# Kernel optimization log

Hardware: AMD Instinct MI355X
Metric: run time of the kernel (lower is better)

Reference implementation:

```python
import jax, jax.numpy as jnp
import numpy as np

N_PATHS, SEQ_LEN = 8192, 512
DATA_DIM, HIDDEN = 2, 128
MIN_VOL, MAX_VOL = 1e-4, 5.0


def setup_inputs() -> dict:
    key = jax.random.key(0)
    ks = jax.random.split(key, 10)
    def w(k, fin, fout, scale=1.0):
        return (jax.random.normal(k, (fin, fout), jnp.float32) * (scale / np.sqrt(fin))).astype(jnp.float32)
    # diffusion output bias init from the torch module: log(exp(target_vol) - 1 + 1e-8)
    gb3_init = float(np.log(np.exp(0.1) - 1.0 + 1e-8))
    return {
        "y0": jax.random.normal(ks[0], (N_PATHS, DATA_DIM), jnp.float32) * 0.1,
        "ts": jnp.arange(SEQ_LEN, dtype=jnp.float32),  # dt = 1.0 between outputs
        "dW": jax.random.normal(ks[1], (SEQ_LEN - 1, N_PATHS, DATA_DIM), jnp.float32),
        "fw1": w(ks[2], DATA_DIM + 1, HIDDEN), "fb1": jnp.zeros((HIDDEN,), jnp.float32),
        "fw2": w(ks[3], HIDDEN, HIDDEN),       "fb2": jnp.zeros((HIDDEN,), jnp.float32),
        "fw3": w(ks[4], HIDDEN, DATA_DIM, 0.02), "fb3": jnp.zeros((DATA_DIM,), jnp.float32),
        "gw1": w(ks[5], DATA_DIM, HIDDEN),     "gb1": jnp.zeros((HIDDEN,), jnp.float32),
        "gw2": w(ks[6], HIDDEN, HIDDEN),       "gb2": jnp.zeros((HIDDEN,), jnp.float32),
        "gw3": w(ks[7], HIDDEN, DATA_DIM, 0.02),
        "gb3": jnp.full((DATA_DIM,), gb3_init, jnp.float32),
    }


def _sde_paths(y0, ts, dW, fw1, fb1, fw2, fb2, fw3, fb3, gw1, gb1, gw2, gb2, gw3, gb3):
    def drift(y):  # f(t, y): MLP on [y, spread]
        spread = y[:, 0:1] - y[:, 1:2]
        h = jnp.concatenate([y, spread], axis=-1)            # [N, D+1]
        h = jax.nn.silu(h @ fw1 + fb1)
        h = jax.nn.silu(h @ fw2 + fb2)
        return h @ fw3 + fb3                                  # [N, D]

    def diffusion(y):  # g(t, y): softplus + clamp
        h = jax.nn.silu(y @ gw1 + gb1)
        h = jax.nn.silu(h @ gw2 + gb2)
        raw = h @ gw3 + gb3
        return jnp.clip(jax.nn.softplus(raw), MIN_VOL, MAX_VOL)  # [N, D]

    dts = ts[1:] - ts[:-1]  # [T-1]

    def step(y, inp):
        dw_std, dt = inp
        dw = dw_std * jnp.sqrt(dt)                 # Brownian increment ~ N(0, dt)
        f = drift(y)
        g, vjp_g = jax.vjp(diffusion, y)
        v = 0.5 * (dw * dw - dt)                   # Milstein weight (Ito)
        corr = vjp_g(v * g)[0]                     # torchsde autograd gdg_prod
        y1 = y + f * dt + g * dw + corr
        return y1, y1

    _, ys = jax.lax.scan(step, y0, (dW, dts))      # ys: [T-1, N, D]
    paths = jnp.concatenate([y0[None], ys], axis=0)  # [T, N, D]
    return jnp.transpose(paths, (1, 0, 2))           # [N, T, D]


def reference(y0, ts, dW, fw1, fb1, fw2, fb2, fw3, fb3, gw1, gb1, gw2, gb2, gw3, gb3):
    return _sde_paths(y0, ts, dW, fw1, fb1, fw2, fb2, fw3, fb3,
                      gw1, gb1, gw2, gb2, gw3, gb3)
```

## Files before the change

kernel.cpp:

```cpp
#include <hip/hip_runtime.h>
#include <math.h>

#define H      128
#define NPATH  8192
#define TLEN   512
#define BP     32
#define NTHR   512

typedef short bf16x8 __attribute__((ext_vector_type(8)));
typedef float f32x4  __attribute__((ext_vector_type(4)));

#define MFMA(a,b,c) __builtin_amdgcn_mfma_f32_16x16x32_bf16((a),(b),(c),0,0,0)

#define O_WF2T  0
#define O_WG2T  (O_WF2T + 32768)
#define O_WG2R  (O_WG2T + 32768)
#define O_BFH   (O_WG2R + 32768)
#define O_BFL   (O_BFH + 8192)
#define O_BGH   (O_BFL + 8192)
#define O_BGL   (O_BGH + 8192)
#define O_PF    (O_BGL + 8192)
#define O_PRAW  (O_PF   + 1024)
#define O_PCORR (O_PRAW + 1024)
#define O_TS    (O_PCORR+ 1024)
#define SMEM_BYTES (O_TS + TLEN*4)

__device__ __forceinline__ float bf2f(unsigned v){ return __uint_as_float(v << 16); }
__device__ __forceinline__ unsigned short f2bf(float f){
  unsigned u = __float_as_uint(f);
  return (unsigned short)((u + 0x7fffu + ((u >> 16) & 1u)) >> 16);
}
__device__ __forceinline__ float ldany(const void* p, long long i, bool isbf){
  return isbf ? bf2f(((const unsigned short*)p)[i]) : ((const float*)p)[i];
}
__device__ __forceinline__ unsigned short ldbf(const void* p, long long i, bool isbf){
  return isbf ? ((const unsigned short*)p)[i] : f2bf(((const float*)p)[i]);
}
__device__ __forceinline__ float fsig(float x){
  return __builtin_amdgcn_rcpf(1.0f + __expf(-x));
}
__device__ __forceinline__ float fsilu(float x){ return x * fsig(x); }
__device__ __forceinline__ float fsilud(float x){
  float s = fsig(x); return s * (1.0f + x * (1.0f - s));
}
__device__ __forceinline__ float fsoftplus(float x){
  if (x > 15.0f) return x;
  return __logf(1.0f + __expf(x));
}
__device__ __forceinline__ void split2(float x, unsigned short& hi, unsigned short& lo){
  unsigned short h = f2bf(x);
  hi = h;
  lo = f2bf(x - bf2f(h));
}
__device__ __forceinline__ int physB(int row, int col){
  return (row << 8) + ((((col >> 3) ^ (row & 15)) << 4) | ((col & 7) << 1));
}
__device__ __forceinline__ bf16x8 ldfrag(const char* base, int row, int col){
  union { uint4 u; bf16x8 b; } v;
  v.u = *(const uint4*)(base + physB(row, col));
  return v.b;
}
__device__ __forceinline__ void st8(char* base, int row, int col, const unsigned short h[8]){
  uint4 u = make_uint4((unsigned)h[0] | ((unsigned)h[1] << 16),
                       (unsigned)h[2] | ((unsigned)h[3] << 16),
                       (unsigned)h[4] | ((unsigned)h[5] << 16),
                       (unsigned)h[6] | ((unsigned)h[7] << 16));
  *(uint4*)(base + physB(row, col)) = u;
}
__device__ __forceinline__ void st4(char* base, int row, int col, const unsigned short h[4]){
  uint2 u = make_uint2((unsigned)h[0] | ((unsigned)h[1] << 16),
                       (unsigned)h[2] | ((unsigned)h[3] << 16));
  *(uint2*)(base + physB(row, col)) = u;
}

__global__ __launch_bounds__(NTHR, 2)
void GeneratorSDE_kernel(const void* __restrict__ y0, const void* __restrict__ ts,
                         const void* __restrict__ dW,
                         const void* __restrict__ fw1, const void* __restrict__ fb1,
                         const void* __restrict__ fw2, const void* __restrict__ fb2,
                         const void* __restrict__ fw3, const void* __restrict__ fb3,
                         const void* __restrict__ gw1, const void* __restrict__ gb1,
                         const void* __restrict__ gw2, const void* __restrict__ gb2,
                         const void* __restrict__ gw3, const void* __restrict__ gb3,
                         void* __restrict__ out)
{
  extern __shared__ char sm[];
  const int tid  = threadIdx.x;
  const int lane = tid & 63;
  const int w    = tid >> 6;
  const int wp   = w >> 1;
  const int nt   = w & 1;
  const int m16  = lane & 15;
  const int q    = lane >> 4;
  const int gpb  = blockIdx.x * BP;
  const int p1   = nt*16 + m16;
  const int gp   = gpb + p1;
  const int k8   = wp*32 + q*8;

  const bool isbf = (((const unsigned*)ts)[1] != 0x3f800000u);

  for (int e = tid; e < H * H; e += NTHR){
    int k = e >> 7, n = e & 127;
    unsigned short fv = ldbf(fw2, e, isbf);
    unsigned short gv = ldbf(gw2, e, isbf);
    *(unsigned short*)(sm + O_WF2T + physB(n, k)) = fv;
    *(unsigned short*)(sm + O_WG2T + physB(n, k)) = gv;
    *(unsigned short*)(sm + O_WG2R + physB(k, n)) = gv;
  }
  for (int e = tid; e < TLEN; e += NTHR)
    ((float*)(sm + O_TS))[e] = ldany(ts, e, isbf);

  float w3f0[8], w3f1[8], w3g0[8], w3g1[8], gw1b0[8], gw1b1[8], gb1b[8], fb2r[8], gb2r[8];
  #pragma unroll
  for (int i = 0; i < 8; ++i){
    int nr = 32*wp + ((i >> 2) << 4) + (q << 2) + (i & 3);
    w3f0[i]  = ldany(fw3, 2*nr + 0, isbf);
    w3f1[i]  = ldany(fw3, 2*nr + 1, isbf);
    w3g0[i]  = ldany(gw3, 2*nr + 0, isbf);
    w3g1[i]  = ldany(gw3, 2*nr + 1, isbf);
    gw1b0[i] = ldany(gw1, nr,       isbf);
    gw1b1[i] = ldany(gw1, H + nr,   isbf);
    gb1b[i]  = ldany(gb1, nr,       isbf);
    fb2r[i]  = ldany(fb2, nr,       isbf);
    gb2r[i]  = ldany(gb2, nr,       isbf);
  }
  float fw1r0[8], fw1r1[8], fw1r2[8], fb1r[8], gw1r0[8], gw1r1[8], gb1r[8];
  #pragma unroll
  for (int kk = 0; kk < 8; ++kk){
    int k = k8 + kk;
    fw1r0[kk] = ldany(fw1, k,       isbf);
    fw1r1[kk] = ldany(fw1, H + k,   isbf);
    fw1r2[kk] = ldany(fw1, 2*H + k, isbf);
    fb1r[kk]  = ldany(fb1, k,       isbf);
    gw1r0[kk] = ldany(gw1, k,       isbf);
    gw1r1[kk] = ldany(gw1, H + k,   isbf);
    gb1r[kk]  = ldany(gb1, k,       isbf);
  }
  const float fb3r0 = ldany(fb3, 0, isbf), fb3r1 = ldany(fb3, 1, isbf);
  const float gb3r0 = ldany(gb3, 0, isbf), gb3r1 = ldany(gb3, 1, isbf);

  float ycur0 = ldany(y0, (long long)gp*2 + 0, isbf);
  float ycur1 = ldany(y0, (long long)gp*2 + 1, isbf);
  if (w < 2 && lane < 16){
    size_t r = (size_t)gp * TLEN;
    if (isbf) ((unsigned*)out)[r] = (unsigned)f2bf(ycur0) | ((unsigned)f2bf(ycur1) << 16);
    else      ((float2*)out)[r]   = make_float2(ycur0, ycur1);
  }
  float2 dwcur;
  {
    long long e = (long long)gp * 2;
    if (isbf){ unsigned u = *(const unsigned*)((const unsigned short*)dW + e);
               dwcur = make_float2(bf2f(u & 0xffffu), bf2f(u >> 16)); }
    else       dwcur = *(const float2*)((const float*)dW + e);
  }
  __syncthreads();

  const float* TSf = (const float*)(sm + O_TS);

  for (int t = 0; t < TLEN - 1; ++t){
    float dt = TSf[t+1] - TSf[t];
    float sqdt = sqrtf(dt);

    float2 dwnext;
    {
      int tn = (t + 1 <= TLEN - 2) ? t + 1 : TLEN - 2;
      long long e = ((long long)tn * NPATH + gp) * 2;
      if (isbf){ unsigned u = *(const unsigned*)((const unsigned short*)dW + e);
                 dwnext = make_float2(bf2f(u & 0xffffu), bf2f(u >> 16)); }
      else       dwnext = *(const float2*)((const float*)dW + e);
    }

    {
      float ysp = ycur0 - ycur1;
      unsigned short fh[8], fl[8], gh[8], gl[8];
      #pragma unroll
      for (int kk = 0; kk < 8; ++kk){
        float hf = fsilu(fb1r[kk] + ycur0*fw1r0[kk] + ycur1*fw1r1[kk] + ysp*fw1r2[kk]);
        float hg = fsilu(gb1r[kk] + ycur0*gw1r0[kk] + ycur1*gw1r1[kk]);
        split2(hf, fh[kk], fl[kk]);
        split2(hg, gh[kk], gl[kk]);
      }
      st8(sm + O_BFH, p1, k8, fh);
      st8(sm + O_BFL, p1, k8, fl);
      st8(sm + O_BGH, p1, k8, gh);
      st8(sm + O_BGL, p1, k8, gl);
    }
    __syncthreads();

    f32x4 accg[2];
    {
      f32x4 accf[2];
      accf[0] = (f32x4)0.f; accf[1] = (f32x4)0.f;
      accg[0] = (f32x4)0.f; accg[1] = (f32x4)0.f;
      #pragma unroll
      for (int kt = 0; kt < 4; ++kt){
        int colk = kt*32 + q*8;
        bf16x8 af0 = ldfrag(sm + O_WF2T, 32*wp + m16,      colk);
        bf16x8 af1 = ldfrag(sm + O_WF2T, 32*wp + 16 + m16, colk);
        bf16x8 bfh = ldfrag(sm + O_BFH, p1, colk);
        bf16x8 bfl = ldfrag(sm + O_BFL, p1, colk);
        accf[0] = MFMA(af0, bfl, accf[0]); accf[0] = MFMA(af0, bfh, accf[0]);
        accf[1] = MFMA(af1, bfl, accf[1]); accf[1] = MFMA(af1, bfh, accf[1]);
        bf16x8 ag0 = ldfrag(sm + O_WG2T, 32*wp + m16,      colk);
        bf16x8 ag1 = ldfrag(sm + O_WG2T, 32*wp + 16 + m16, colk);
        bf16x8 bgh = ldfrag(sm + O_BGH, p1, colk);
        bf16x8 bgl = ldfrag(sm + O_BGL, p1, colk);
        accg[0] = MFMA(ag0, bgl, accg[0]); accg[0] = MFMA(ag0, bgh, accg[0]);
        accg[1] = MFMA(ag1, bgl, accg[1]); accg[1] = MFMA(ag1, bgh, accg[1]);
      }
      float pf0 = 0, pf1 = 0, pr0 = 0, pr1 = 0;
      #pragma unroll
      for (int mi = 0; mi < 2; ++mi)
        #pragma unroll
        for (int r = 0; r < 4; ++r){
          int i = mi*4 + r;
          float vf = fsilu(accf[mi][r] + fb2r[i]);
          pf0 += vf * w3f0[i];
          pf1 += vf * w3f1[i];
          float zg = accg[mi][r] + gb2r[i];
          accg[mi][r] = zg;
          float vg = fsilu(zg);
          pr0 += vg * w3g0[i];
          pr1 += vg * w3g1[i];
        }
      pf0 += __shfl_xor(pf0, 16, 64); pf0 += __shfl_xor(pf0, 32, 64);
      pf1 += __shfl_xor(pf1, 16, 64); pf1 += __shfl_xor(pf1, 32, 64);
      pr0 += __shfl_xor(pr0, 16, 64); pr0 += __shfl_xor(pr0, 32, 64);
      pr1 += __shfl_xor(pr1, 16, 64); pr1 += __shfl_xor(pr1, 32, 64);
      if (lane < 16){
        *(float2*)(sm + O_PF   + (wp*32 + p1)*8) = make_float2(pf0, pf1);
        *(float2*)(sm + O_PRAW + (wp*32 + p1)*8) = make_float2(pr0, pr1);
      }
    }
    __syncthreads();

    float g0, g1, dw0, dw1, cr0, cr1;
    {
      float raw0 = gb3r0, raw1 = gb3r1;
      #pragma unroll
      for (int w2 = 0; w2 < 4; ++w2){
        float2 v = *(const float2*)(sm + O_PRAW + (w2*32 + p1)*8);
        raw0 += v.x; raw1 += v.y;
      }
      dw0 = dwcur.x * sqdt; dw1 = dwcur.y * sqdt;
      float vv0 = 0.5f*(dw0*dw0 - dt), vv1 = 0.5f*(dw1*dw1 - dt);
      float sp0 = fsoftplus(raw0), sp1 = fsoftplus(raw1);
      g0 = fminf(fmaxf(sp0, 1e-4f), 5.0f);
      g1 = fminf(fmaxf(sp1, 1e-4f), 5.0f);
      float m0 = (sp0 > 1e-4f && sp0 < 5.0f) ? 1.0f : 0.0f;
      float m1 = (sp1 > 1e-4f && sp1 < 5.0f) ? 1.0f : 0.0f;
      cr0 = vv0 * (g0 * fsig(raw0) * m0);
      cr1 = vv1 * (g1 * fsig(raw1) * m1);
    }

    #pragma unroll
    for (int mi = 0; mi < 2; ++mi){
      unsigned short hi[4], lo[4];
      #pragma unroll
      for (int r = 0; r < 4; ++r){
        int i = mi*4 + r;
        float c2 = (cr0 * w3g0[i] + cr1 * w3g1[i]) * fsilud(accg[mi][r]);
        split2(c2, hi[r], lo[r]);
      }
      st4(sm + O_BFH, p1, 32*wp + 16*mi + q*4, hi);
      st4(sm + O_BFL, p1, 32*wp + 16*mi + q*4, lo);
    }
    __syncthreads();

    {
      f32x4 accc[2];
      accc[0] = (f32x4)0.f; accc[1] = (f32x4)0.f;
      #pragma unroll
      for (int kt = 0; kt < 4; ++kt){
        int colk = kt*32 + q*8;
        bf16x8 a0 = ldfrag(sm + O_WG2R, 32*wp + m16,      colk);
        bf16x8 a1 = ldfrag(sm + O_WG2R, 32*wp + 16 + m16, colk);
        bf16x8 bh = ldfrag(sm + O_BFH, p1, colk);
        bf16x8 bl = ldfrag(sm + O_BFL, p1, colk);
        accc[0] = MFMA(a0, bl, accc[0]); accc[0] = MFMA(a0, bh, accc[0]);
        accc[1] = MFMA(a1, bl, accc[1]); accc[1] = MFMA(a1, bh, accc[1]);
      }
      float pc0 = 0, pc1 = 0;
      #pragma unroll
      for (int mi = 0; mi < 2; ++mi)
        #pragma unroll
        for (int r = 0; r < 4; ++r){
          int i = mi*4 + r;
          float z1 = gb1b[i] + ycur0*gw1b0[i] + ycur1*gw1b1[i];
          float u  = accc[mi][r] * fsilud(z1);
          pc0 += u * gw1b0[i];
          pc1 += u * gw1b1[i];
        }
      pc0 += __shfl_xor(pc0, 16, 64); pc0 += __shfl_xor(pc0, 32, 64);
      pc1 += __shfl_xor(pc1, 16, 64); pc1 += __shfl_xor(pc1, 32, 64);
      if (lane < 16)
        *(float2*)(sm + O_PCORR + (wp*32 + p1)*8) = make_float2(pc0, pc1);
    }
    __syncthreads();

    {
      float f0 = fb3r0, f1 = fb3r1, c0 = 0.f, c1 = 0.f;
      #pragma unroll
      for (int w2 = 0; w2 < 4; ++w2){
        float2 a = *(const float2*)(sm + O_PF    + (w2*32 + p1)*8);
        float2 b = *(const float2*)(sm + O_PCORR + (w2*32 + p1)*8);
        f0 += a.x; f1 += a.y; c0 += b.x; c1 += b.y;
      }
      ycur0 += f0*dt + g0*dw0 + c0;
      ycur1 += f1*dt + g1*dw1 + c1;
      if (w < 2 && lane < 16){
        size_t r = (size_t)gp * TLEN + (t + 1);
        if (isbf) ((unsigned*)out)[r] = (unsigned)f2bf(ycur0) | ((unsigned)f2bf(ycur1) << 16);
        else      ((float2*)out)[r]   = make_float2(ycur0, ycur1);
      }
      dwcur = dwnext;
    }
  }
}

extern "C" void kernel_launch(void* const* d_in, const int* in_sizes, int n_in,
                              void* d_out, int out_size, void* d_ws, size_t ws_size,
                              hipStream_t stream)
{
  (void)in_sizes; (void)n_in; (void)out_size; (void)d_ws; (void)ws_size;
  hipFuncSetAttribute((const void*)GeneratorSDE_kernel,
                      hipFuncAttributeMaxDynamicSharedMemorySize, SMEM_BYTES);
  GeneratorSDE_kernel<<<dim3(NPATH / BP), dim3(NTHR), SMEM_BYTES, stream>>>(
      d_in[0], d_in[1], d_in[2],
      d_in[3], d_in[4], d_in[5], d_in[6], d_in[7], d_in[8],
      d_in[9], d_in[10], d_in[11], d_in[12], d_in[13], d_in[14],
      d_out);
}
```

Before: 2.060 ms.

## Double threads per block so each wave owns 16 hidden units

The block grows from 512 to 1024 threads (16 waves), so each wave now computes a single 16-row MFMA tile of the hidden dimension instead of two. This halves the per-wave serial MFMA and elementwise work in each time step. Cross-wave partial sums move to a padded per-path layout and are reduced with a cheaper two-load plus shuffle pattern. The spread input is folded algebraically into the first-layer weights, and the sigmoid is reused for the silu derivative. In exchange, each barrier now has to synchronize twice as many waves, and the launch bounds are raised.

```diff
diff --git a/kernel.cpp b/kernel.cpp
--- a/kernel.cpp
+++ b/kernel.cpp
@@ -5,7 +5,8 @@
 #define NPATH  8192
 #define TLEN   512
 #define BP     32
-#define NTHR   512
+#define NTHR   1024
+#define PSTR   9
 
 typedef short bf16x8 __attribute__((ext_vector_type(8)));
 typedef float f32x4  __attribute__((ext_vector_type(4)));
@@ -20,9 +21,9 @@
 #define O_BGH   (O_BFL + 8192)
 #define O_BGL   (O_BGH + 8192)
 #define O_PF    (O_BGL + 8192)
-#define O_PRAW  (O_PF   + 1024)
-#define O_PCORR (O_PRAW + 1024)
-#define O_TS    (O_PCORR+ 1024)
+#define O_PRAW  (O_PF   + 32*PSTR*8)
+#define O_PCORR (O_PRAW + 32*PSTR*8)
+#define O_TS    (O_PCORR+ 32*PSTR*8)
 #define SMEM_BYTES (O_TS + TLEN*4)
 
 __device__ __forceinline__ float bf2f(unsigned v){ return __uint_as_float(v << 16); }
@@ -60,20 +61,13 @@
   v.u = *(const uint4*)(base + physB(row, col));
   return v.b;
 }
-__device__ __forceinline__ void st8(char* base, int row, int col, const unsigned short h[8]){
-  uint4 u = make_uint4((unsigned)h[0] | ((unsigned)h[1] << 16),
-                       (unsigned)h[2] | ((unsigned)h[3] << 16),
-                       (unsigned)h[4] | ((unsigned)h[5] << 16),
-                       (unsigned)h[6] | ((unsigned)h[7] << 16));
-  *(uint4*)(base + physB(row, col)) = u;
-}
 __device__ __forceinline__ void st4(char* base, int row, int col, const unsigned short h[4]){
   uint2 u = make_uint2((unsigned)h[0] | ((unsigned)h[1] << 16),
                        (unsigned)h[2] | ((unsigned)h[3] << 16));
   *(uint2*)(base + physB(row, col)) = u;
 }
 
-__global__ __launch_bounds__(NTHR, 2)
+__global__ __launch_bounds__(NTHR, 4)
 void GeneratorSDE_kernel(const void* __restrict__ y0, const void* __restrict__ ts,
                          const void* __restrict__ dW,
                          const void* __restrict__ fw1, const void* __restrict__ fb1,
@@ -95,7 +89,7 @@
   const int gpb  = blockIdx.x * BP;
   const int p1   = nt*16 + m16;
   const int gp   = gpb + p1;
-  const int k8   = wp*32 + q*8;
+  const int k4   = wp*16 + q*4;
 
   const bool isbf = (((const unsigned*)ts)[1] != 0x3f800000u);
 
@@ -110,10 +104,10 @@
   for (int e = tid; e < TLEN; e += NTHR)
     ((float*)(sm + O_TS))[e] = ldany(ts, e, isbf);
 
-  float w3f0[8], w3f1[8], w3g0[8], w3g1[8], gw1b0[8], gw1b1[8], gb1b[8], fb2r[8], gb2r[8];
+  float w3f0[4], w3f1[4], w3g0[4], w3g1[4], gw1b0[4], gw1b1[4], gb1b[4], fb2r[4], gb2r[4];
   #pragma unroll
-  for (int i = 0; i < 8; ++i){
-    int nr = 32*wp + ((i >> 2) << 4) + (q << 2) + (i & 3);
+  for (int i = 0; i < 4; ++i){
+    int nr = 16*wp + (q << 2) + i;
     w3f0[i]  = ldany(fw3, 2*nr + 0, isbf);
     w3f1[i]  = ldany(fw3, 2*nr + 1, isbf);
     w3g0[i]  = ldany(gw3, 2*nr + 0, isbf);
@@ -124,17 +118,19 @@
     fb2r[i]  = ldany(fb2, nr,       isbf);
     gb2r[i]  = ldany(gb2, nr,       isbf);
   }
-  float fw1r0[8], fw1r1[8], fw1r2[8], fb1r[8], gw1r0[8], gw1r1[8], gb1r[8];
+  float fw1a[4], fw1b[4], fb1r[4], gw1r0[4], gw1r1[4], gb1r[4];
   #pragma unroll
-  for (int kk = 0; kk < 8; ++kk){
-    int k = k8 + kk;
-    fw1r0[kk] = ldany(fw1, k,       isbf);
-    fw1r1[kk] = ldany(fw1, H + k,   isbf);
-    fw1r2[kk] = ldany(fw1, 2*H + k, isbf);
-    fb1r[kk]  = ldany(fb1, k,       isbf);
-    gw1r0[kk] = ldany(gw1, k,       isbf);
-    gw1r1[kk] = ldany(gw1, H + k,   isbf);
-    gb1r[kk]  = ldany(gb1, k,       isbf);
+  for (int kk = 0; kk < 4; ++kk){
+    int k = k4 + kk;
+    float r0 = ldany(fw1, k,       isbf);
+    float r1 = ldany(fw1, H + k,   isbf);
+    float r2 = ldany(fw1, 2*H + k, isbf);
+    fw1a[kk]  = r0 + r2;
+    fw1b[kk]  = r1 - r2;
+    fb1r[kk]  = ldany(fb1, k,     isbf);
+    gw1r0[kk] = ldany(gw1, k,     isbf);
+    gw1r1[kk] = ldany(gw1, H + k, isbf);
+    gb1r[kk]  = ldany(gb1, k,     isbf);
   }
   const float fb3r0 = ldany(fb3, 0, isbf), fb3r1 = ldany(fb3, 1, isbf);
   const float gb3r0 = ldany(gb3, 0, isbf), gb3r1 = ldany(gb3, 1, isbf);
@@ -171,77 +167,70 @@
     }
 
     {
-      float ysp = ycur0 - ycur1;
-      unsigned short fh[8], fl[8], gh[8], gl[8];
-      #pragma unroll
-      for (int kk = 0; kk < 8; ++kk){
-        float hf = fsilu(fb1r[kk] + ycur0*fw1r0[kk] + ycur1*fw1r1[kk] + ysp*fw1r2[kk]);
+      unsigned short fh[4], fl[4], gh[4], gl[4];
+      #pragma unroll
+      for (int kk = 0; kk < 4; ++kk){
+        float hf = fsilu(fb1r[kk] + ycur0*fw1a[kk]  + ycur1*fw1b[kk]);
         float hg = fsilu(gb1r[kk] + ycur0*gw1r0[kk] + ycur1*gw1r1[kk]);
         split2(hf, fh[kk], fl[kk]);
         split2(hg, gh[kk], gl[kk]);
       }
-      st8(sm + O_BFH, p1, k8, fh);
-      st8(sm + O_BFL, p1, k8, fl);
-      st8(sm + O_BGH, p1, k8, gh);
-      st8(sm + O_BGL, p1, k8, gl);
+      st4(sm + O_BFH, p1, k4, fh);
+      st4(sm + O_BFL, p1, k4, fl);
+      st4(sm + O_BGH, p1, k4, gh);
+      st4(sm + O_BGL, p1, k4, gl);
     }
     __syncthreads();
 
-    f32x4 accg[2];
-    {
-      f32x4 accf[2];
-      accf[0] = (f32x4)0.f; accf[1] = (f32x4)0.f;
-      accg[0] = (f32x4)0.f; accg[1] = (f32x4)0.f;
+    f32x4 accg;
+    float sgr[4];
+    {
+      f32x4 accf = (f32x4)0.f; accg = (f32x4)0.f;
       #pragma unroll
       for (int kt = 0; kt < 4; ++kt){
         int colk = kt*32 + q*8;
-        bf16x8 af0 = ldfrag(sm + O_WF2T, 32*wp + m16,      colk);
-        bf16x8 af1 = ldfrag(sm + O_WF2T, 32*wp + 16 + m16, colk);
+        bf16x8 af  = ldfrag(sm + O_WF2T, 16*wp + m16, colk);
         bf16x8 bfh = ldfrag(sm + O_BFH, p1, colk);
         bf16x8 bfl = ldfrag(sm + O_BFL, p1, colk);
-        accf[0] = MFMA(af0, bfl, accf[0]); accf[0] = MFMA(af0, bfh, accf[0]);
-        accf[1] = MFMA(af1, bfl, accf[1]); accf[1] = MFMA(af1, bfh, accf[1]);
-        bf16x8 ag0 = ldfrag(sm + O_WG2T, 32*wp + m16,      colk);
-        bf16x8 ag1 = ldfrag(sm + O_WG2T, 32*wp + 16 + m16, colk);
+        accf = MFMA(af, bfl, accf); accf = MFMA(af, bfh, accf);
+        bf16x8 ag  = ldfrag(sm + O_WG2T, 16*wp + m16, colk);
         bf16x8 bgh = ldfrag(sm + O_BGH, p1, colk);
         bf16x8 bgl = ldfrag(sm + O_BGL, p1, colk);
-        accg[0] = MFMA(ag0, bgl, accg[0]); accg[0] = MFMA(ag0, bgh, accg[0]);
-        accg[1] = MFMA(ag1, bgl, accg[1]); accg[1] = MFMA(ag1, bgh, accg[1]);
+        accg = MFMA(ag, bgl, accg); accg = MFMA(ag, bgh, accg);
       }
       float pf0 = 0, pf1 = 0, pr0 = 0, pr1 = 0;
       #pragma unroll
-      for (int mi = 0; mi < 2; ++mi)
-        #pragma unroll
-        for (int r = 0; r < 4; ++r){
-          int i = mi*4 + r;
-          float vf = fsilu(accf[mi][r] + fb2r[i]);
-          pf0 += vf * w3f0[i];
-          pf1 += vf * w3f1[i];
-          float zg = accg[mi][r] + gb2r[i];
-          accg[mi][r] = zg;
-          float vg = fsilu(zg);
-          pr0 += vg * w3g0[i];
-          pr1 += vg * w3g1[i];
-        }
+      for (int r = 0; r < 4; ++r){
+        float vf = fsilu(accf[r] + fb2r[r]);
+        pf0 += vf * w3f0[r];
+        pf1 += vf * w3f1[r];
+        float zg = accg[r] + gb2r[r];
+        accg[r] = zg;
+        float s = fsig(zg);
+        sgr[r] = s;
+        float vg = zg * s;
+        pr0 += vg * w3g0[r];
+        pr1 += vg * w3g1[r];
+      }
       pf0 += __shfl_xor(pf0, 16, 64); pf0 += __shfl_xor(pf0, 32, 64);
       pf1 += __shfl_xor(pf1, 16, 64); pf1 += __shfl_xor(pf1, 32, 64);
       pr0 += __shfl_xor(pr0, 16, 64); pr0 += __shfl_xor(pr0, 32, 64);
       pr1 += __shfl_xor(pr1, 16, 64); pr1 += __shfl_xor(pr1, 32, 64);
       if (lane < 16){
-        *(float2*)(sm + O_PF   + (wp*32 + p1)*8) = make_float2(pf0, pf1);
-        *(float2*)(sm + O_PRAW + (wp*32 + p1)*8) = make_float2(pr0, pr1);
+        *(float2*)(sm + O_PF   + (p1*PSTR + wp)*8) = make_float2(pf0, pf1);
+        *(float2*)(sm + O_PRAW + (p1*PSTR + wp)*8) = make_float2(pr0, pr1);
       }
     }
     __syncthreads();
 
     float g0, g1, dw0, dw1, cr0, cr1;
     {
-      float raw0 = gb3r0, raw1 = gb3r1;
-      #pragma unroll
-      for (int w2 = 0; w2 < 4; ++w2){
-        float2 v = *(const float2*)(sm + O_PRAW + (w2*32 + p1)*8);
-        raw0 += v.x; raw1 += v.y;
-      }
+      float2 a = *(const float2*)(sm + O_PRAW + (p1*PSTR + 2*q    )*8);
+      float2 b = *(const float2*)(sm + O_PRAW + (p1*PSTR + 2*q + 1)*8);
+      float raw0 = a.x + b.x, raw1 = a.y + b.y;
+      raw0 += __shfl_xor(raw0, 16, 64); raw0 += __shfl_xor(raw0, 32, 64);
+      raw1 += __shfl_xor(raw1, 16, 64); raw1 += __shfl_xor(raw1, 32, 64);
+      raw0 += gb3r0; raw1 += gb3r1;
       dw0 = dwcur.x * sqdt; dw1 = dwcur.y * sqdt;
       float vv0 = 0.5f*(dw0*dw0 - dt), vv1 = 0.5f*(dw1*dw1 - dt);
       float sp0 = fsoftplus(raw0), sp1 = fsoftplus(raw1);
@@ -253,59 +242,56 @@
       cr1 = vv1 * (g1 * fsig(raw1) * m1);
     }
 
-    #pragma unroll
-    for (int mi = 0; mi < 2; ++mi){
+    {
       unsigned short hi[4], lo[4];
       #pragma unroll
       for (int r = 0; r < 4; ++r){
-        int i = mi*4 + r;
-        float c2 = (cr0 * w3g0[i] + cr1 * w3g1[i]) * fsilud(accg[mi][r]);
+        float sd = sgr[r] * (1.0f + accg[r] * (1.0f - sgr[r]));
+        float c2 = (cr0 * w3g0[r] + cr1 * w3g1[r]) * sd;
         split2(c2, hi[r], lo[r]);
       }
-      st4(sm + O_BFH, p1, 32*wp + 16*mi + q*4, hi);
-      st4(sm + O_BFL, p1, 32*wp + 16*mi + q*4, lo);
+      st4(sm + O_BFH, p1, 16*wp + (q << 2), hi);
+      st4(sm + O_BFL, p1, 16*wp + (q << 2), lo);
     }
     __syncthreads();
 
     {
-      f32x4 accc[2];
-      accc[0] = (f32x4)0.f; accc[1] = (f32x4)0.f;
+      f32x4 accc = (f32x4)0.f;
       #pragma unroll
       for (int kt = 0; kt < 4; ++kt){
         int colk = kt*32 + q*8;
-        bf16x8 a0 = ldfrag(sm + O_WG2R, 32*wp + m16,      colk);
-        bf16x8 a1 = ldfrag(sm + O_WG2R, 32*wp + 16 + m16, colk);
+        bf16x8 a0 = ldfrag(sm + O_WG2R, 16*wp + m16, colk);
         bf16x8 bh = ldfrag(sm + O_BFH, p1, colk);
         bf16x8 bl = ldfrag(sm + O_BFL, p1, colk);
-        accc[0] = MFMA(a0, bl, accc[0]); accc[0] = MFMA(a0, bh, accc[0]);
-        accc[1] = MFMA(a1, bl, accc[1]); accc[1] = MFMA(a1, bh, accc[1]);
+        accc = MFMA(a0, bl, accc); accc = MFMA(a0, bh, accc);
       }
       float pc0 = 0, pc1 = 0;
       #pragma unroll
-      for (int mi = 0; mi < 2; ++mi)
-        #pragma unroll
-        for (int r = 0; r < 4; ++r){
-          int i = mi*4 + r;
-          float z1 = gb1b[i] + ycur0*gw1b0[i] + ycur1*gw1b1[i];
-          float u  = accc[mi][r] * fsilud(z1);
-          pc0 += u * gw1b0[i];
-          pc1 += u * gw1b1[i];
-        }
+      for (int r = 0; r < 4; ++r){
+        float z1 = gb1b[r] + ycur0*gw1b0[r] + ycur1*gw1b1[r];
+        float u  = accc[r] * fsilud(z1);
+        pc0 += u * gw1b0[r];
+        pc1 += u * gw1b1[r];
+      }
       pc0 += __shfl_xor(pc0, 16, 64); pc0 += __shfl_xor(pc0, 32, 64);
       pc1 += __shfl_xor(pc1, 16, 64); pc1 += __shfl_xor(pc1, 32, 64);
       if (lane < 16)
-        *(float2*)(sm + O_PCORR + (wp*32 + p1)*8) = make_float2(pc0, pc1);
+        *(float2*)(sm + O_PCORR + (p1*PSTR + wp)*8) = make_float2(pc0, pc1);
     }
     __syncthreads();
 
     {
-      float f0 = fb3r0, f1 = fb3r1, c0 = 0.f, c1 = 0.f;
-      #pragma unroll
-      for (int w2 = 0; w2 < 4; ++w2){
-        float2 a = *(const float2*)(sm + O_PF    + (w2*32 + p1)*8);
-        float2 b = *(const float2*)(sm + O_PCORR + (w2*32 + p1)*8);
-        f0 += a.x; f1 += a.y; c0 += b.x; c1 += b.y;
-      }
+      float2 a0 = *(const float2*)(sm + O_PF    + (p1*PSTR + 2*q    )*8);
+      float2 a1 = *(const float2*)(sm + O_PF    + (p1*PSTR + 2*q + 1)*8);
+      float2 b0 = *(const float2*)(sm + O_PCORR + (p1*PSTR + 2*q    )*8);
+      float2 b1 = *(const float2*)(sm + O_PCORR + (p1*PSTR + 2*q + 1)*8);
+      float f0 = a0.x + a1.x, f1 = a0.y + a1.y;
+      float c0 = b0.x + b1.x, c1 = b0.y + b1.y;
+      f0 += __shfl_xor(f0, 16, 64); f0 += __shfl_xor(f0, 32, 64);
+      f1 += __shfl_xor(f1, 16, 64); f1 += __shfl_xor(f1, 32, 64);
+      c0 += __shfl_xor(c0, 16, 64); c0 += __shfl_xor(c0, 32, 64);
+      c1 += __shfl_xor(c1, 16, 64); c1 += __shfl_xor(c1, 32, 64);
+      f0 += fb3r0; f1 += fb3r1;
       ycur0 += f0*dt + g0*dw0 + c0;
       ycur1 += f1*dt + g1*dw1 + c1;
       if (w < 2 && lane < 16){
```

Result: slower. 5.162 ms (+150.6%).

## Keep layer-2 weight fragments in registers and use packed bf16 conversion

Applied to the files above, without the earlier changes.

Moves the fw2/gw2 MFMA A-fragments (forward, transposed, and reverse copies) out of LDS into per-thread registers loaded once before the time loop, so each step no longer rereads weights from shared memory. LDS use shrinks from about 100KB to about 36KB. The hi/lo bf16 split now uses the v_cvt_pk_bf16_f32 instruction on pairs of values, and the spread input is folded into the first-layer weights. The register arrays add 96 VGPRs per thread, which may cause spills or lower occupancy under launch_bounds(512,2). The hardware conversion may round differently from the old manual rounding.

```diff
diff --git a/kernel.cpp b/kernel.cpp
--- a/kernel.cpp
+++ b/kernel.cpp
@@ -12,14 +12,11 @@
 
 #define MFMA(a,b,c) __builtin_amdgcn_mfma_f32_16x16x32_bf16((a),(b),(c),0,0,0)
 
-#define O_WF2T  0
-#define O_WG2T  (O_WF2T + 32768)
-#define O_WG2R  (O_WG2T + 32768)
-#define O_BFH   (O_WG2R + 32768)
-#define O_BFL   (O_BFH + 8192)
-#define O_BGH   (O_BFL + 8192)
-#define O_BGL   (O_BGH + 8192)
-#define O_PF    (O_BGL + 8192)
+#define O_BFH   0
+#define O_BFL   8192
+#define O_BGH   16384
+#define O_BGL   24576
+#define O_PF    32768
 #define O_PRAW  (O_PF   + 1024)
 #define O_PCORR (O_PRAW + 1024)
 #define O_TS    (O_PCORR+ 1024)
@@ -47,10 +44,8 @@
   if (x > 15.0f) return x;
   return __logf(1.0f + __expf(x));
 }
-__device__ __forceinline__ void split2(float x, unsigned short& hi, unsigned short& lo){
-  unsigned short h = f2bf(x);
-  hi = h;
-  lo = f2bf(x - bf2f(h));
+__device__ __forceinline__ unsigned cvtpk(float a, float b){
+  unsigned r; asm("v_cvt_pk_bf16_f32 %0, %1, %2" : "=v"(r) : "v"(a), "v"(b)); return r;
 }
 __device__ __forceinline__ int physB(int row, int col){
   return (row << 8) + ((((col >> 3) ^ (row & 15)) << 4) | ((col & 7) << 1));
@@ -60,17 +55,26 @@
   v.u = *(const uint4*)(base + physB(row, col));
   return v.b;
 }
-__device__ __forceinline__ void st8(char* base, int row, int col, const unsigned short h[8]){
-  uint4 u = make_uint4((unsigned)h[0] | ((unsigned)h[1] << 16),
-                       (unsigned)h[2] | ((unsigned)h[3] << 16),
-                       (unsigned)h[4] | ((unsigned)h[5] << 16),
-                       (unsigned)h[6] | ((unsigned)h[7] << 16));
-  *(uint4*)(base + physB(row, col)) = u;
-}
-__device__ __forceinline__ void st4(char* base, int row, int col, const unsigned short h[4]){
-  uint2 u = make_uint2((unsigned)h[0] | ((unsigned)h[1] << 16),
-                       (unsigned)h[2] | ((unsigned)h[3] << 16));
-  *(uint2*)(base + physB(row, col)) = u;
+__device__ __forceinline__ void split8_store(char* baseH, char* baseL, int row, int col, const float v[8]){
+  unsigned h[4], l[4];
+  #pragma unroll
+  for (int i = 0; i < 4; ++i) h[i] = cvtpk(v[2*i], v[2*i+1]);
+  #pragma unroll
+  for (int i = 0; i < 4; ++i){
+    float h0 = __uint_as_float(h[i] << 16);
+    float h1 = __uint_as_float(h[i] & 0xffff0000u);
+    l[i] = cvtpk(v[2*i] - h0, v[2*i+1] - h1);
+  }
+  *(uint4*)(baseH + physB(row, col)) = make_uint4(h[0], h[1], h[2], h[3]);
+  *(uint4*)(baseL + physB(row, col)) = make_uint4(l[0], l[1], l[2], l[3]);
+}
+__device__ __forceinline__ void split4_store(char* baseH, char* baseL, int row, int col, const float v[4]){
+  unsigned h0 = cvtpk(v[0], v[1]), h1 = cvtpk(v[2], v[3]);
+  float a0 = __uint_as_float(h0 << 16), a1 = __uint_as_float(h0 & 0xffff0000u);
+  float a2 = __uint_as_float(h1 << 16), a3 = __uint_as_float(h1 & 0xffff0000u);
+  unsigned l0 = cvtpk(v[0] - a0, v[1] - a1), l1 = cvtpk(v[2] - a2, v[3] - a3);
+  *(uint2*)(baseH + physB(row, col)) = make_uint2(h0, h1);
+  *(uint2*)(baseL + physB(row, col)) = make_uint2(l0, l1);
 }
 
 __global__ __launch_bounds__(NTHR, 2)
@@ -99,16 +103,23 @@
 
   const bool isbf = (((const unsigned*)ts)[1] != 0x3f800000u);
 
-  for (int e = tid; e < H * H; e += NTHR){
-    int k = e >> 7, n = e & 127;
-    unsigned short fv = ldbf(fw2, e, isbf);
-    unsigned short gv = ldbf(gw2, e, isbf);
-    *(unsigned short*)(sm + O_WF2T + physB(n, k)) = fv;
-    *(unsigned short*)(sm + O_WG2T + physB(n, k)) = gv;
-    *(unsigned short*)(sm + O_WG2R + physB(k, n)) = gv;
-  }
   for (int e = tid; e < TLEN; e += NTHR)
     ((float*)(sm + O_TS))[e] = ldany(ts, e, isbf);
+
+  bf16x8 aF[2][4], aG[2][4], aR[2][4];
+  #pragma unroll
+  for (int mi = 0; mi < 2; ++mi)
+    #pragma unroll
+    for (int kt = 0; kt < 4; ++kt){
+      int row = 32*wp + 16*mi + m16;
+      #pragma unroll
+      for (int j = 0; j < 8; ++j){
+        int col = kt*32 + q*8 + j;
+        aF[mi][kt][j] = (short)ldbf(fw2, (long long)col*H + row, isbf);
+        aG[mi][kt][j] = (short)ldbf(gw2, (long long)col*H + row, isbf);
+        aR[mi][kt][j] = (short)ldbf(gw2, (long long)row*H + col, isbf);
+      }
+    }
 
   float w3f0[8], w3f1[8], w3g0[8], w3g1[8], gw1b0[8], gw1b1[8], gb1b[8], fb2r[8], gb2r[8];
   #pragma unroll
@@ -124,17 +135,17 @@
     fb2r[i]  = ldany(fb2, nr,       isbf);
     gb2r[i]  = ldany(gb2, nr,       isbf);
   }
-  float fw1r0[8], fw1r1[8], fw1r2[8], fb1r[8], gw1r0[8], gw1r1[8], gb1r[8];
+  float fw1a[8], fw1b[8], fb1r[8], gw1r0[8], gw1r1[8], gb1r[8];
   #pragma unroll
   for (int kk = 0; kk < 8; ++kk){
     int k = k8 + kk;
-    fw1r0[kk] = ldany(fw1, k,       isbf);
-    fw1r1[kk] = ldany(fw1, H + k,   isbf);
-    fw1r2[kk] = ldany(fw1, 2*H + k, isbf);
-    fb1r[kk]  = ldany(fb1, k,       isbf);
-    gw1r0[kk] = ldany(gw1, k,       isbf);
-    gw1r1[kk] = ldany(gw1, H + k,   isbf);
-    gb1r[kk]  = ldany(gb1, k,       isbf);
+    float r0 = ldany(fw1, k, isbf), r1 = ldany(fw1, H + k, isbf), r2 = ldany(fw1, 2*H + k, isbf);
+    fw1a[kk]  = r0 + r2;
+    fw1b[kk]  = r1 - r2;
+    fb1r[kk]  = ldany(fb1, k,     isbf);
+    gw1r0[kk] = ldany(gw1, k,     isbf);
+    gw1r1[kk] = ldany(gw1, H + k, isbf);
+    gb1r[kk]  = ldany(gb1, k,     isbf);
   }
   const float fb3r0 = ldany(fb3, 0, isbf), fb3r1 = ldany(fb3, 1, isbf);
   const float gb3r0 = ldany(gb3, 0, isbf), gb3r1 = ldany(gb3, 1, isbf);
@@ -171,19 +182,14 @@
     }
 
     {
-      float ysp = ycur0 - ycur1;
-      unsigned short fh[8], fl[8], gh[8], gl[8];
+      float hf[8], hg[8];
       #pragma unroll
       for (int kk = 0; kk < 8; ++kk){
-        float hf = fsilu(fb1r[kk] + ycur0*fw1r0[kk] + ycur1*fw1r1[kk] + ysp*fw1r2[kk]);
-        float hg = fsilu(gb1r[kk] + ycur0*gw1r0[kk] + ycur1*gw1r1[kk]);
-        split2(hf, fh[kk], fl[kk]);
-        split2(hg, gh[kk], gl[kk]);
-      }
-      st8(sm + O_BFH, p1, k8, fh);
-      st8(sm + O_BFL, p1, k8, fl);
-      st8(sm + O_BGH, p1, k8, gh);
-      st8(sm + O_BGL, p1, k8, gl);
+        hf[kk] = fsilu(fb1r[kk] + ycur0*fw1a[kk]  + ycur1*fw1b[kk]);
+        hg[kk] = fsilu(gb1r[kk] + ycur0*gw1r0[kk] + ycur1*gw1r1[kk]);
+      }
+      split8_store(sm + O_BFH, sm + O_BFL, p1, k8, hf);
+      split8_store(sm + O_BGH, sm + O_BGL, p1, k8, hg);
     }
     __syncthreads();
 
@@ -195,18 +201,14 @@
       #pragma unroll
       for (int kt = 0; kt < 4; ++kt){
         int colk = kt*32 + q*8;
-        bf16x8 af0 = ldfrag(sm + O_WF2T, 32*wp + m16,      colk);
-        bf16x8 af1 = ldfrag(sm + O_WF2T, 32*wp + 16 + m16, colk);
         bf16x8 bfh = ldfrag(sm + O_BFH, p1, colk);
         bf16x8 bfl = ldfrag(sm + O_BFL, p1, colk);
-        accf[0] = MFMA(af0, bfl, accf[0]); accf[0] = MFMA(af0, bfh, accf[0]);
-        accf[1] = MFMA(af1, bfl, accf[1]); accf[1] = MFMA(af1, bfh, accf[1]);
-        bf16x8 ag0 = ldfrag(sm + O_WG2T, 32*wp + m16,      colk);
-        bf16x8 ag1 = ldfrag(sm + O_WG2T, 32*wp + 16 + m16, colk);
         bf16x8 bgh = ldfrag(sm + O_BGH, p1, colk);
         bf16x8 bgl = ldfrag(sm + O_BGL, p1, colk);
-        accg[0] = MFMA(ag0, bgl, accg[0]); accg[0] = MFMA(ag0, bgh, accg[0]);
-        accg[1] = MFMA(ag1, bgl, accg[1]); accg[1] = MFMA(ag1, bgh, accg[1]);
+        accf[0] = MFMA(aF[0][kt], bfl, accf[0]); accf[0] = MFMA(aF[0][kt], bfh, accf[0]);
+        accf[1] = MFMA(aF[1][kt], bfl, accf[1]); accf[1] = MFMA(aF[1][kt], bfh, accf[1]);
+        accg[0] = MFMA(aG[0][kt], bgl, accg[0]); accg[0] = MFMA(aG[0][kt], bgh, accg[0]);
+        accg[1] = MFMA(aG[1][kt], bgl, accg[1]); accg[1] = MFMA(aG[1][kt], bgh, accg[1]);
       }
       float pf0 = 0, pf1 = 0, pr0 = 0, pr1 = 0;
       #pragma unroll
@@ -255,15 +257,13 @@
 
     #pragma unroll
     for (int mi = 0; mi < 2; ++mi){
-      unsigned short hi[4], lo[4];
+      float c2[4];
       #pragma unroll
       for (int r = 0; r < 4; ++r){
         int i = mi*4 + r;
-        float c2 = (cr0 * w3g0[i] + cr1 * w3g1[i]) * fsilud(accg[mi][r]);
-        split2(c2, hi[r], lo[r]);
-      }
-      st4(sm + O_BFH, p1, 32*wp + 16*mi + q*4, hi);
-      st4(sm + O_BFL, p1, 32*wp + 16*mi + q*4, lo);
+        c2[r] = (cr0 * w3g0[i] + cr1 * w3g1[i]) * fsilud(accg[mi][r]);
+      }
+      split4_store(sm + O_BFH, sm + O_BFL, p1, 32*wp + 16*mi + q*4, c2);
     }
     __syncthreads();
 
@@ -273,12 +273,10 @@
       #pragma unroll
       for (int kt = 0; kt < 4; ++kt){
         int colk = kt*32 + q*8;
-        bf16x8 a0 = ldfrag(sm + O_WG2R, 32*wp + m16,      colk);
-        bf16x8 a1 = ldfrag(sm + O_WG2R, 32*wp + 16 + m16, colk);
         bf16x8 bh = ldfrag(sm + O_BFH, p1, colk);
         bf16x8 bl = ldfrag(sm + O_BFL, p1, colk);
-        accc[0] = MFMA(a0, bl, accc[0]); accc[0] = MFMA(a0, bh, accc[0]);
-        accc[1] = MFMA(a1, bl, accc[1]); accc[1] = MFMA(a1, bh, accc[1]);
+        accc[0] = MFMA(aR[0][kt], bl, accc[0]); accc[0] = MFMA(aR[0][kt], bh, accc[0]);
+        accc[1] = MFMA(aR[1][kt], bl, accc[1]); accc[1] = MFMA(aR[1][kt], bh, accc[1]);
       }
       float pc0 = 0, pc1 = 0;
       #pragma unroll
```

After: 3.593 ms. +74.4%, slower.
